# Optimization experiments

Hardware: AMD Instinct MI355X
Metric: run time of the kernel (lower is better)

The kernel has to match this reference:

```python
import jax, jax.numpy as jnp
import numpy as np

LAMDA = 0.5

def setup_inputs() -> dict:
    key = jax.random.key(0)
    k1, k2 = jax.random.split(key)
    X_set = jax.random.normal(k1, (8192, 128), dtype=jnp.float32)
    Y_set = jax.random.randint(k2, (8192,), 0, 100, dtype=jnp.int64)
    return {"X_set": X_set, "Y_set": Y_set}

def _pairwise_euclidean(X):
    # X: [N, D] -> D: [N, N] euclidean distances (torch.cdist p=2)
    sq_norms = jnp.sum(X * X, axis=1)  # [N]
    sq = sq_norms[:, None] + sq_norms[None, :] - 2.0 * (X @ X.T)  # [N, N]
    sq = jnp.maximum(sq, 0.0)
    # safe sqrt (zero diagonal) to stay grad-safe under jit
    pos = sq > 0.0
    return jnp.where(pos, jnp.sqrt(jnp.where(pos, sq, 1.0)), 0.0)

def reference(X_set, Y_set):
    X = X_set.reshape(X_set.shape[0], -1)
    D = _pairwise_euclidean(X)  # [N, N]
    same = Y_set[:, None] == Y_set[None, :]  # [N, N] bool
    # Class loop in original == sum of within-class distances (incl. zero diag)
    # minus lamda * sum over all ordered cross-class pairs (each unordered
    # cross pair is counted once for each of its two classes -> full mask).
    pos_sum = jnp.sum(jnp.where(same, D, 0.0))
    neg_sum = jnp.sum(jnp.where(same, 0.0, D))
    return pos_sum - LAMDA * neg_sum
```

## Files before the change

kernel.cpp:

```cpp
#include <hip/hip_runtime.h>

#define N_ROWS 8192
#define DIM    128
#define BM     128
#define BK     64
#define NBLK   (N_ROWS / BM)
#define NTRI   (NBLK * (NBLK + 1) / 2)

typedef _Float16 half4 __attribute__((ext_vector_type(4)));
typedef _Float16 half8 __attribute__((ext_vector_type(8)));
typedef float    f32x16 __attribute__((ext_vector_type(16)));

__global__ __launch_bounds__(256)
void prep_kernel(const float* __restrict__ X,
                 _Float16* __restrict__ Xhi, _Float16* __restrict__ Xlo,
                 float* __restrict__ norms)
{
    const int g = blockIdx.x * 256 + threadIdx.x;
    const float4 v = ((const float4*)X)[g];
    half4 h, l;
    h.x = (_Float16)v.x; l.x = (_Float16)(v.x - (float)h.x);
    h.y = (_Float16)v.y; l.y = (_Float16)(v.y - (float)h.y);
    h.z = (_Float16)v.z; l.z = (_Float16)(v.z - (float)h.z);
    h.w = (_Float16)v.w; l.w = (_Float16)(v.w - (float)h.w);
    *(half4*)(Xhi + (size_t)g * 4) = h;
    *(half4*)(Xlo + (size_t)g * 4) = l;

    float s = fmaf(v.x, v.x, fmaf(v.y, v.y, fmaf(v.z, v.z, v.w * v.w)));
    #pragma unroll
    for (int off = 1; off <= 16; off <<= 1) s += __shfl_xor(s, off);
    if ((threadIdx.x & 31) == 0) norms[g >> 5] = s;
}

__global__ __launch_bounds__(256)
void pairsum_mfma(const _Float16* __restrict__ Xhi, const _Float16* __restrict__ Xlo,
                  const float* __restrict__ norms, const int* __restrict__ Y,
                  double* __restrict__ gsum)
{
    const int kb = blockIdx.x;
    int bi = (int)((129.0f - sqrtf(fmaf(-8.0f, (float)kb, 129.0f * 129.0f))) * 0.5f);
    while ((bi + 1) * (129 - (bi + 1)) / 2 <= kb) ++bi;
    while (bi * (129 - bi) / 2 > kb) --bi;
    const int bj = bi + (kb - bi * (129 - bi) / 2);
    const int i0 = bi * BM, j0 = bj * BM;

    const int tid  = threadIdx.x;
    const int lane = tid & 63;
    const int w    = tid >> 6;
    const int wy   = w >> 1;
    const int wx   = w & 1;
    const int lr   = lane & 31;
    const int lh   = lane >> 5;

    __shared__ __align__(16) char tile[65536];
    const int AH = 0, AL = 16384, BH = 32768, BL = 49152;
    __shared__ float nI[BM], nJ[BM];
    __shared__ int   yI[BM], yJ[BM];
    __shared__ double wsum[4];

    if (tid < BM) { nI[tid] = norms[i0 + tid]; yI[tid] = Y[i0 + tid]; }
    else { const int r = tid & (BM - 1); nJ[r] = norms[j0 + r]; yJ[r] = Y[j0 + r]; }

    f32x16 acc[2][2];
    #pragma unroll
    for (int m = 0; m < 2; ++m)
        #pragma unroll
        for (int n = 0; n < 2; ++n)
            #pragma unroll
            for (int r = 0; r < 16; ++r)
                acc[m][n][r] = 0.0f;

    #pragma unroll
    for (int c = 0; c < 2; ++c) {
        const int kc = c * BK;
        __syncthreads();
        #pragma unroll
        for (int p = 0; p < 4; ++p) {
            const int g2  = p * 256 + tid;
            const int row = g2 >> 3;
            const int kk  = g2 & 7;
            const int off = row * 128 + (((kk ^ (row & 7)) << 4));
            const size_t ga = (size_t)(i0 + row) * DIM + kc + kk * 8;
            const size_t gb = (size_t)(j0 + row) * DIM + kc + kk * 8;
            *(half8*)(tile + AH + off) = *(const half8*)(Xhi + ga);
            *(half8*)(tile + AL + off) = *(const half8*)(Xlo + ga);
            *(half8*)(tile + BH + off) = *(const half8*)(Xhi + gb);
            *(half8*)(tile + BL + off) = *(const half8*)(Xlo + gb);
        }
        __syncthreads();
        #pragma unroll
        for (int ks = 0; ks < 4; ++ks) {
            const int kk16 = ks * 2 + lh;
            half8 ah[2], al[2], bh[2], bl[2];
            #pragma unroll
            for (int m = 0; m < 2; ++m) {
                const int ar = wy * 64 + m * 32 + lr;
                const int ao = ar * 128 + (((kk16 ^ (ar & 7)) << 4));
                ah[m] = *(const half8*)(tile + AH + ao);
                al[m] = *(const half8*)(tile + AL + ao);
                const int br = wx * 64 + m * 32 + lr;
                const int bo = br * 128 + (((kk16 ^ (br & 7)) << 4));
                bh[m] = *(const half8*)(tile + BH + bo);
                bl[m] = *(const half8*)(tile + BL + bo);
            }
            #pragma unroll
            for (int m = 0; m < 2; ++m)
                #pragma unroll
                for (int n = 0; n < 2; ++n) {
                    acc[m][n] = __builtin_amdgcn_mfma_f32_32x32x16_f16(ah[m], bh[n], acc[m][n], 0, 0, 0);
                    acc[m][n] = __builtin_amdgcn_mfma_f32_32x32x16_f16(ah[m], bl[n], acc[m][n], 0, 0, 0);
                    acc[m][n] = __builtin_amdgcn_mfma_f32_32x32x16_f16(al[m], bh[n], acc[m][n], 0, 0, 0);
                }
        }
    }

    float s = 0.0f;
    float nJv[2]; int yJv[2];
    #pragma unroll
    for (int n = 0; n < 2; ++n) {
        const int lj = wx * 64 + n * 32 + lr;
        nJv[n] = nJ[lj]; yJv[n] = yJ[lj];
    }
    #pragma unroll
    for (int m = 0; m < 2; ++m) {
        #pragma unroll
        for (int r = 0; r < 16; ++r) {
            const int rowin = (r & 3) + 8 * (r >> 2) + 4 * lh;
            const int li = wy * 64 + m * 32 + rowin;
            const float ni = nI[li];
            const int   yi = yI[li];
            const int   gi = i0 + li;
            #pragma unroll
            for (int n = 0; n < 2; ++n) {
                const int gj = j0 + wx * 64 + n * 32 + lr;
                float sq = fmaf(-2.0f, acc[m][n][r], ni + nJv[n]);
                sq = fmaxf(sq, 0.0f);
                const float d = __builtin_amdgcn_sqrtf(sq);
                if (gi < gj) s = fmaf((yi == yJv[n]) ? 1.0f : -0.5f, d, s);
            }
        }
    }

    #pragma unroll
    for (int off = 32; off > 0; off >>= 1) s += __shfl_down(s, off);
    if (lane == 0) wsum[w] = (double)s;
    __syncthreads();
    if (tid == 0) atomicAdd(gsum, wsum[0] + wsum[1] + wsum[2] + wsum[3]);
}

__global__ void finalize_kernel(const double* __restrict__ gsum, float* __restrict__ out)
{
    out[0] = (float)(2.0 * gsum[0]);
}

#define LDSPAD 4
#define LDB (BM + LDSPAD)
__global__ __launch_bounds__(256)
void pairsum_valu(const float* __restrict__ X, const int* __restrict__ Y,
                  double* __restrict__ gsum)
{
    const int bj = blockIdx.x, bi = blockIdx.y;
    if (bi > bj) return;
    const int tid = threadIdx.x;
    const int i0 = bi * BM, j0 = bj * BM;
    __shared__ float As[32][LDB], Bs[32][LDB];
    __shared__ float nI[BM], nJ[BM];
    __shared__ int yI[BM], yJ[BM];
    __shared__ double wsum[4];
    {
        const int r = tid & (BM - 1);
        const bool isJ = tid >= BM;
        const int row = (isJ ? j0 : i0) + r;
        const float4* p = (const float4*)(X + (size_t)row * DIM);
        float s = 0.f;
        #pragma unroll
        for (int q = 0; q < DIM / 4; ++q) {
            float4 v = p[q];
            s = fmaf(v.x, v.x, s); s = fmaf(v.y, v.y, s);
            s = fmaf(v.z, v.z, s); s = fmaf(v.w, v.w, s);
        }
        if (isJ) { nJ[r] = s; yJ[r] = Y[row]; }
        else     { nI[r] = s; yI[r] = Y[row]; }
    }
    float dot[8][8];
    #pragma unroll
    for (int m = 0; m < 8; ++m)
        #pragma unroll
        for (int n = 0; n < 8; ++n) dot[m][n] = 0.f;
    const int tx = tid & 15, ty = tid >> 4;
    for (int kc = 0; kc < DIM; kc += 32) {
        __syncthreads();
        #pragma unroll
        for (int p = 0; p < 4; ++p) {
            const int s2 = p * 256 + tid;
            const int row = s2 >> 3, kg = s2 & 7;
            const float4 va = *(const float4*)(X + (size_t)(i0 + row) * DIM + kc + kg * 4);
            const float4 vb = *(const float4*)(X + (size_t)(j0 + row) * DIM + kc + kg * 4);
            As[kg*4+0][row] = va.x; As[kg*4+1][row] = va.y;
            As[kg*4+2][row] = va.z; As[kg*4+3][row] = va.w;
            Bs[kg*4+0][row] = vb.x; Bs[kg*4+1][row] = vb.y;
            Bs[kg*4+2][row] = vb.z; Bs[kg*4+3][row] = vb.w;
        }
        __syncthreads();
        #pragma unroll
        for (int k = 0; k < 32; ++k) {
            float a[8], b[8];
            *(float4*)&a[0] = *(const float4*)&As[k][ty*8];
            *(float4*)&a[4] = *(const float4*)&As[k][ty*8+4];
            *(float4*)&b[0] = *(const float4*)&Bs[k][tx*8];
            *(float4*)&b[4] = *(const float4*)&Bs[k][tx*8+4];
            #pragma unroll
            for (int m = 0; m < 8; ++m)
                #pragma unroll
                for (int n = 0; n < 8; ++n)
                    dot[m][n] = fmaf(a[m], b[n], dot[m][n]);
        }
    }
    float s = 0.f;
    const int ib = ty * 8, jb = tx * 8;
    #pragma unroll
    for (int m = 0; m < 8; ++m) {
        const int gi = i0 + ib + m;
        const float ni = nI[ib + m];
        const int yi = yI[ib + m];
        #pragma unroll
        for (int n = 0; n < 8; ++n) {
            const int gj = j0 + jb + n;
            float sq = fmaf(-2.f, dot[m][n], ni + nJ[jb + n]);
            sq = fmaxf(sq, 0.f);
            const float d = __builtin_amdgcn_sqrtf(sq);
            if (gi < gj) s = fmaf((yi == yJ[jb + n]) ? 1.0f : -0.5f, d, s);
        }
    }
    #pragma unroll
    for (int off = 32; off > 0; off >>= 1) s += __shfl_down(s, off);
    const int lane = tid & 63, wid = tid >> 6;
    if (lane == 0) wsum[wid] = (double)s;
    __syncthreads();
    if (tid == 0) atomicAdd(gsum, wsum[0] + wsum[1] + wsum[2] + wsum[3]);
}

extern "C" void kernel_launch(void* const* d_in, const int* in_sizes, int n_in,
                              void* d_out, int out_size, void* d_ws, size_t ws_size,
                              hipStream_t stream)
{
    const float* X = (const float*)d_in[0];
    const int*   Y = (const int*)d_in[1];
    float* out = (float*)d_out;

    const size_t OFF_NORM = 64;
    const size_t OFF_XHI  = OFF_NORM + (size_t)N_ROWS * 4;
    const size_t OFF_XLO  = OFF_XHI + (size_t)N_ROWS * DIM * 2;
    const size_t REQ      = OFF_XLO + (size_t)N_ROWS * DIM * 2;

    double* gsum = (double*)d_ws;
    hipMemsetAsync(d_ws, 0, sizeof(double), stream);

    if (ws_size >= REQ) {
        float*     norms = (float*)((char*)d_ws + OFF_NORM);
        _Float16*  Xhi   = (_Float16*)((char*)d_ws + OFF_XHI);
        _Float16*  Xlo   = (_Float16*)((char*)d_ws + OFF_XLO);
        prep_kernel<<<(N_ROWS * DIM / 4) / 256, 256, 0, stream>>>(X, Xhi, Xlo, norms);
        pairsum_mfma<<<NTRI, 256, 0, stream>>>(Xhi, Xlo, norms, Y, gsum);
    } else {
        dim3 grid(NBLK, NBLK);
        pairsum_valu<<<grid, 256, 0, stream>>>(X, Y, gsum);
    }
    finalize_kernel<<<1, 1, 0, stream>>>(gsum, out);
}
```

Measured before the change: 118.4 us.

## Pre-swizzle fp16 hi/lo tiles and double-buffer LDS with direct global-to-LDS loads

The prep kernel now writes X's fp16 hi/lo split into a blob already laid out per row-block and K-phase in the swizzled LDS format, with hi and lo interleaved in each row. The pairwise kernel copies these blobs straight into LDS with global_load_lds, using two buffers and four K-phases so that loading the next phase overlaps MFMA work on the current one. This removes the register round-trip and exposed load latency of the old two-chunk staging loop. The cost is hand-managed vmcnt waits and barriers, which are fragile if the compiler reorders loads.

```diff
diff --git a/kernel.cpp b/kernel.cpp
--- a/kernel.cpp
+++ b/kernel.cpp
@@ -3,39 +3,61 @@
 #define N_ROWS 8192
 #define DIM    128
 #define BM     128
-#define BK     64
 #define NBLK   (N_ROWS / BM)
 #define NTRI   (NBLK * (NBLK + 1) / 2)
 
-typedef _Float16 half4 __attribute__((ext_vector_type(4)));
+#define BLOB_PER_RB   65536
+#define BLOB_PER_PH   16384
+
 typedef _Float16 half8 __attribute__((ext_vector_type(8)));
 typedef float    f32x16 __attribute__((ext_vector_type(16)));
 
+typedef const __attribute__((address_space(1))) unsigned int glb_uint;
+typedef __attribute__((address_space(3))) unsigned int lds_uint;
+
+__device__ inline void gload_lds16(const void* g, void* l)
+{
+    __builtin_amdgcn_global_load_lds((glb_uint*)(uintptr_t)g,
+                                     (lds_uint*)(uintptr_t)l, 16, 0, 0);
+}
+
 __global__ __launch_bounds__(256)
-void prep_kernel(const float* __restrict__ X,
-                 _Float16* __restrict__ Xhi, _Float16* __restrict__ Xlo,
-                 float* __restrict__ norms)
-{
-    const int g = blockIdx.x * 256 + threadIdx.x;
-    const float4 v = ((const float4*)X)[g];
-    half4 h, l;
-    h.x = (_Float16)v.x; l.x = (_Float16)(v.x - (float)h.x);
-    h.y = (_Float16)v.y; l.y = (_Float16)(v.y - (float)h.y);
-    h.z = (_Float16)v.z; l.z = (_Float16)(v.z - (float)h.z);
-    h.w = (_Float16)v.w; l.w = (_Float16)(v.w - (float)h.w);
-    *(half4*)(Xhi + (size_t)g * 4) = h;
-    *(half4*)(Xlo + (size_t)g * 4) = l;
-
-    float s = fmaf(v.x, v.x, fmaf(v.y, v.y, fmaf(v.z, v.z, v.w * v.w)));
-    #pragma unroll
-    for (int off = 1; off <= 16; off <<= 1) s += __shfl_xor(s, off);
-    if ((threadIdx.x & 31) == 0) norms[g >> 5] = s;
+void prep_tiled(const float* __restrict__ X, char* __restrict__ blob,
+                float* __restrict__ norms)
+{
+    const int t   = blockIdx.x * 256 + threadIdx.x;
+    const int gg  = t & 3;
+    const int p   = (t >> 2) & 3;
+    const int row = t >> 4;
+
+    const float4* src = (const float4*)(X + (size_t)row * DIM + p * 32 + gg * 8);
+    const float4 v0 = src[0], v1 = src[1];
+    const float xs[8] = {v0.x, v0.y, v0.z, v0.w, v1.x, v1.y, v1.z, v1.w};
+
+    half8 h, l;
+    float ns = 0.0f;
+    #pragma unroll
+    for (int i = 0; i < 8; ++i) {
+        const float x = xs[i];
+        const _Float16 hh = (_Float16)x;
+        h[i] = hh;
+        l[i] = (_Float16)(x - (float)hh);
+        ns = fmaf(x, x, ns);
+    }
+
+    const int rb = row >> 7, r = row & 127;
+    char* base = blob + (size_t)rb * BLOB_PER_RB + p * BLOB_PER_PH + r * 128;
+    *(half8*)(base + (((gg    ) ^ (r & 7)) << 4)) = h;
+    *(half8*)(base + (((gg + 4) ^ (r & 7)) << 4)) = l;
+
+    #pragma unroll
+    for (int off = 1; off <= 8; off <<= 1) ns += __shfl_xor(ns, off);
+    if ((t & 15) == 0) norms[row] = ns;
 }
 
 __global__ __launch_bounds__(256)
-void pairsum_mfma(const _Float16* __restrict__ Xhi, const _Float16* __restrict__ Xlo,
-                  const float* __restrict__ norms, const int* __restrict__ Y,
-                  double* __restrict__ gsum)
+void pairsum_mfma(const char* __restrict__ blob, const float* __restrict__ norms,
+                  const int* __restrict__ Y, double* __restrict__ gsum)
 {
     const int kb = blockIdx.x;
     int bi = (int)((129.0f - sqrtf(fmaf(-8.0f, (float)kb, 129.0f * 129.0f))) * 0.5f);
@@ -53,13 +75,27 @@
     const int lh   = lane >> 5;
 
     __shared__ __align__(16) char tile[65536];
-    const int AH = 0, AL = 16384, BH = 32768, BL = 49152;
     __shared__ float nI[BM], nJ[BM];
     __shared__ int   yI[BM], yJ[BM];
     __shared__ double wsum[4];
 
     if (tid < BM) { nI[tid] = norms[i0 + tid]; yI[tid] = Y[i0 + tid]; }
     else { const int r = tid & (BM - 1); nJ[r] = norms[j0 + r]; yJ[r] = Y[j0 + r]; }
+    __syncthreads();
+
+    const char* Ablob = blob + (size_t)bi * BLOB_PER_RB;
+    const char* Bblob = blob + (size_t)bj * BLOB_PER_RB;
+
+    auto STAGE = [&](int p, int s) {
+        const char* gA = Ablob + p * BLOB_PER_PH + tid * 16;
+        const char* gB = Bblob + p * BLOB_PER_PH + tid * 16;
+        char* lA = tile + s * 32768 + tid * 16;
+        #pragma unroll
+        for (int q = 0; q < 4; ++q) {
+            gload_lds16(gA + q * 4096, lA + q * 4096);
+            gload_lds16(gB + q * 4096, lA + 16384 + q * 4096);
+        }
+    };
 
     f32x16 acc[2][2];
     #pragma unroll
@@ -70,38 +106,32 @@
             for (int r = 0; r < 16; ++r)
                 acc[m][n][r] = 0.0f;
 
-    #pragma unroll
-    for (int c = 0; c < 2; ++c) {
-        const int kc = c * BK;
-        __syncthreads();
-        #pragma unroll
-        for (int p = 0; p < 4; ++p) {
-            const int g2  = p * 256 + tid;
-            const int row = g2 >> 3;
-            const int kk  = g2 & 7;
-            const int off = row * 128 + (((kk ^ (row & 7)) << 4));
-            const size_t ga = (size_t)(i0 + row) * DIM + kc + kk * 8;
-            const size_t gb = (size_t)(j0 + row) * DIM + kc + kk * 8;
-            *(half8*)(tile + AH + off) = *(const half8*)(Xhi + ga);
-            *(half8*)(tile + AL + off) = *(const half8*)(Xlo + ga);
-            *(half8*)(tile + BH + off) = *(const half8*)(Xhi + gb);
-            *(half8*)(tile + BL + off) = *(const half8*)(Xlo + gb);
-        }
-        __syncthreads();
-        #pragma unroll
-        for (int ks = 0; ks < 4; ++ks) {
-            const int kk16 = ks * 2 + lh;
+    STAGE(0, 0);
+    STAGE(1, 1);
+
+    #pragma unroll
+    for (int p = 0; p < 4; ++p) {
+        if (p < 3) asm volatile("s_waitcnt vmcnt(8)" ::: "memory");
+        else       asm volatile("s_waitcnt vmcnt(0)" ::: "memory");
+        __builtin_amdgcn_s_barrier();
+        __builtin_amdgcn_sched_barrier(0);
+
+        const char* Ab = tile + ((p & 1) ? 32768 : 0);
+        const char* Bb = Ab + 16384;
+        #pragma unroll
+        for (int ks = 0; ks < 2; ++ks) {
+            const int g = ks * 2 + lh;
             half8 ah[2], al[2], bh[2], bl[2];
             #pragma unroll
             for (int m = 0; m < 2; ++m) {
                 const int ar = wy * 64 + m * 32 + lr;
-                const int ao = ar * 128 + (((kk16 ^ (ar & 7)) << 4));
-                ah[m] = *(const half8*)(tile + AH + ao);
-                al[m] = *(const half8*)(tile + AL + ao);
+                const int ao = ar * 128 + (((g ^ (ar & 7))) << 4);
+                ah[m] = *(const half8*)(Ab + ao);
+                al[m] = *(const half8*)(Ab + (ao ^ 64));
                 const int br = wx * 64 + m * 32 + lr;
-                const int bo = br * 128 + (((kk16 ^ (br & 7)) << 4));
-                bh[m] = *(const half8*)(tile + BH + bo);
-                bl[m] = *(const half8*)(tile + BL + bo);
+                const int bo = br * 128 + (((g ^ (br & 7))) << 4);
+                bh[m] = *(const half8*)(Bb + bo);
+                bl[m] = *(const half8*)(Bb + (bo ^ 64));
             }
             #pragma unroll
             for (int m = 0; m < 2; ++m)
@@ -112,6 +142,10 @@
                     acc[m][n] = __builtin_amdgcn_mfma_f32_32x32x16_f16(al[m], bh[n], acc[m][n], 0, 0, 0);
                 }
         }
+
+        __builtin_amdgcn_sched_barrier(0);
+        __builtin_amdgcn_s_barrier();
+        if (p + 2 < 4) STAGE(p + 2, p & 1);
     }
 
     float s = 0.0f;
@@ -248,20 +282,18 @@
     const int*   Y = (const int*)d_in[1];
     float* out = (float*)d_out;
 
-    const size_t OFF_NORM = 64;
-    const size_t OFF_XHI  = OFF_NORM + (size_t)N_ROWS * 4;
-    const size_t OFF_XLO  = OFF_XHI + (size_t)N_ROWS * DIM * 2;
-    const size_t REQ      = OFF_XLO + (size_t)N_ROWS * DIM * 2;
+    const size_t OFF_BLOB = 64;
+    const size_t OFF_NORM = OFF_BLOB + (size_t)NBLK * BLOB_PER_RB;
+    const size_t REQ      = OFF_NORM + (size_t)N_ROWS * 4;
 
     double* gsum = (double*)d_ws;
     hipMemsetAsync(d_ws, 0, sizeof(double), stream);
 
     if (ws_size >= REQ) {
-        float*     norms = (float*)((char*)d_ws + OFF_NORM);
-        _Float16*  Xhi   = (_Float16*)((char*)d_ws + OFF_XHI);
-        _Float16*  Xlo   = (_Float16*)((char*)d_ws + OFF_XLO);
-        prep_kernel<<<(N_ROWS * DIM / 4) / 256, 256, 0, stream>>>(X, Xhi, Xlo, norms);
-        pairsum_mfma<<<NTRI, 256, 0, stream>>>(Xhi, Xlo, norms, Y, gsum);
+        char*  blob  = (char*)d_ws + OFF_BLOB;
+        float* norms = (float*)((char*)d_ws + OFF_NORM);
+        prep_tiled<<<(N_ROWS * 16) / 256, 256, 0, stream>>>(X, blob, norms);
+        pairsum_mfma<<<NTRI, 256, 0, stream>>>(blob, norms, Y, gsum);
     } else {
         dim3 grid(NBLK, NBLK);
         pairsum_valu<<<grid, 256, 0, stream>>>(X, Y, gsum);
```

After: 105.5 us. 10.9% less time.
